# Kernel tuning notes

Hardware: AMD Instinct MI355X
Metric: run time of the kernel (lower is better)

Reference implementation:

```python
import jax, jax.numpy as jnp
import numpy as np

B, S, H = 2, 2048, 2048
HQ, HKV, DK, DV = 32, 8, 64, 64
G = HQ // HKV  # queries per kv group
SCALE = 1.0 / DK ** 0.5


def setup_inputs() -> dict:
    key = jax.random.key(0)
    k1, k2, k3, k4 = jax.random.split(key, 4)
    qkv_out = HQ * DK + HKV * (DK + DV)
    x = jax.random.normal(k1, (B, S, H), dtype=jnp.float32)
    Wqkv = jax.random.normal(k2, (H, qkv_out), dtype=jnp.float32) * (1.0 / np.sqrt(H))
    Wout = jax.random.normal(k3, (HQ * DV, H), dtype=jnp.float32) * (1.0 / np.sqrt(HQ * DV))
    b_out = jax.random.normal(k4, (H,), dtype=jnp.float32) * 0.01
    # causal mask [B, 1, S, S]; mask==0 positions are disallowed
    mask = jnp.broadcast_to(jnp.tril(jnp.ones((S, S), dtype=jnp.int32)), (B, 1, S, S))
    return {"x": x, "Wqkv": Wqkv, "Wout": Wout, "b_out": b_out, "mask": mask}


def reference(x, Wqkv, Wout, b_out, mask):
    # fused QKV projection (bias=False)
    qkv = x @ Wqkv  # [B, S, HQ*DK + HKV*(DK+DV)]
    tq, tk = HQ * DK, HKV * DK
    Q = qkv[..., :tq].reshape(B, S, HKV, G, DK)          # [B,S,n,g,d]
    K = qkv[..., tq:tq + tk].reshape(B, S, HKV, DK)       # [B,S,n,d]
    V = qkv[..., tq + tk:].reshape(B, S, HKV, DV)         # [B,S,n,e]
    # scores: [B, n(kv heads), g(group), s(query), t(key)]
    scores = jnp.einsum('bsngd,btnd->bngst', Q, K) * SCALE
    # mask [B,1,S,S] -> broadcast over n,g as [B,1,1,S,S]
    m = mask[:, :, None, :, :]
    scores = jnp.where(m == 0, -jnp.inf, scores)
    probs = jax.nn.softmax(scores, axis=-1)  # dropout p=0 -> identity
    attn = jnp.einsum('bngst,btne->bsnge', probs, V)      # [B,S,n,g,e]
    out = attn.reshape(B, S, HQ * DV) @ Wout + b_out       # [B,S,H]
    return out
```

## Files before the change

### kernel.cpp

```cpp
#include <hip/hip_runtime.h>

#define SEQ    2048
#define HDIM   2048
#define QKV_LD 3072
#define K_BASE 2048
#define V_BASE 2560
#define ATT_SCALE 0.125f
#define SM_MAX 20.0f
#define QK_MUL 0.18033688f
#define ZINIT  -28.8539008f

typedef __bf16 bf16x8 __attribute__((ext_vector_type(8)));
typedef float  f32x4  __attribute__((ext_vector_type(4)));
typedef float  f32x16 __attribute__((ext_vector_type(16)));
typedef unsigned short u16x8 __attribute__((ext_vector_type(8)));
typedef unsigned       u32x4 __attribute__((ext_vector_type(4)));

__device__ __forceinline__ void async_copy16(void* lds, const void* g) {
  __builtin_amdgcn_global_load_lds(
      (const __attribute__((address_space(1))) unsigned*)g,
      (__attribute__((address_space(3))) unsigned*)lds, 16, 0, 0);
}

__device__ __forceinline__ unsigned cvtpk(float lo, float hi) {
  unsigned r;
  asm("v_cvt_pk_bf16_f32 %0, %1, %2" : "=v"(r) : "v"(lo), "v"(hi));
  return r;
}
__device__ __forceinline__ void pl32swap(unsigned& a, unsigned& b) {
  asm("v_permlane32_swap_b32 %0, %1" : "+v"(a), "+v"(b));
}

__global__ void detect_dtype(const unsigned* __restrict__ p0,
                             const unsigned* __restrict__ p1,
                             const unsigned* __restrict__ p2,
                             const unsigned* __restrict__ p3,
                             int* __restrict__ flags) {
  const unsigned* ptrs[4] = {p0, p1, p2, p3};
  const int lane = threadIdx.x;
#pragma unroll
  for (int i = 0; i < 4; ++i) {
    int cnt = 0;
#pragma unroll
    for (int j = 0; j < 8; ++j) {
      unsigned w = ptrs[i][lane * 8 + j];
      unsigned e = (w >> 7) & 0xFF;
      cnt += (e >= 90 && e <= 160) ? 1 : 0;
    }
    for (int off = 32; off; off >>= 1) cnt += __shfl_down(cnt, off);
    if (lane == 0) flags[i] = (cnt < 350) ? 1 : 0;
  }
  if (lane == 0) flags[4] = 0;
}

__global__ __launch_bounds__(256) void cast_f32_bf16(const float* __restrict__ s,
                                                     __bf16* __restrict__ d) {
  const size_t i = ((size_t)blockIdx.x * 256 + threadIdx.x) * 8;
  float4 a = *(const float4*)(s + i);
  float4 b = *(const float4*)(s + i + 4);
  bf16x8 o;
  o[0] = (__bf16)a.x; o[1] = (__bf16)a.y; o[2] = (__bf16)a.z; o[3] = (__bf16)a.w;
  o[4] = (__bf16)b.x; o[5] = (__bf16)b.y; o[6] = (__bf16)b.z; o[7] = (__bf16)b.w;
  *(bf16x8*)(d + i) = o;
}

__global__ __launch_bounds__(256) void transpose_cast(const float* __restrict__ W,
                                                      __bf16* __restrict__ WT,
                                                      int K, int N) {
  __shared__ float T[64][68];
  const int tid = threadIdx.x;
  const int kb = blockIdx.y * 64, nb = blockIdx.x * 64;
  const int r = tid >> 2, cq = tid & 3;
  const float* src = W + (size_t)(kb + r) * N + nb + cq * 16;
  float4 f0 = ((const float4*)src)[0];
  float4 f1 = ((const float4*)src)[1];
  float4 f2 = ((const float4*)src)[2];
  float4 f3 = ((const float4*)src)[3];
  *(float4*)&T[r][cq * 16 + 0]  = f0;
  *(float4*)&T[r][cq * 16 + 4]  = f1;
  *(float4*)&T[r][cq * 16 + 8]  = f2;
  *(float4*)&T[r][cq * 16 + 12] = f3;
  __syncthreads();
  __bf16* dst = WT + (size_t)(nb + r) * K + kb + cq * 16;
  bf16x8 o0, o1;
#pragma unroll
  for (int j = 0; j < 8; ++j) o0[j] = (__bf16)T[cq * 16 + j][r];
#pragma unroll
  for (int j = 0; j < 8; ++j) o1[j] = (__bf16)T[cq * 16 + 8 + j][r];
  *(bf16x8*)dst = o0;
  *(bf16x8*)(dst + 8) = o1;
}

#define QA_ELE (128 * 64)
#define QB_ELE (192 * 64)

template <typename OutT>
__global__ __launch_bounds__(512, 4) void gemm128x192(const __bf16* __restrict__ A,
                                                      const __bf16* __restrict__ Bt,
                                                      const float* __restrict__ bias,
                                                      OutT* __restrict__ C,
                                                      int M, int N, int K) {
  extern __shared__ __align__(16) __bf16 smem[];
  __bf16* Asm = smem;
  __bf16* Bsm = smem + 2 * QA_ELE;

  const int tid = threadIdx.x;
  const int w = tid >> 6, lane = tid & 63;
  const int lr = lane & 15, lg = lane >> 4;
  const int wm = w >> 2, wn = w & 3;
  const int bid = blockIdx.x;
  const int cpx = gridDim.x >> 3;
  const int swz = (bid & 7) * cpx + (bid >> 3);
  const int nx = N / 192;
  const int m0 = (swz / nx) * 128, n0 = (swz % nx) * 192;
  const int KT = K >> 6;

  const int lrow = lane >> 3;
  const int lc8  = ((lane & 7) ^ lrow) * 8;

  f32x4 acc[4][3];
#pragma unroll
  for (int a = 0; a < 4; ++a)
#pragma unroll
    for (int b = 0; b < 3; ++b) acc[a][b] = (f32x4){0.f, 0.f, 0.f, 0.f};

  bf16x8 af[4][2], bf[3][2];

  const __bf16* gA = A + (size_t)m0 * K;
  const __bf16* gB = Bt + (size_t)n0 * K;

  auto stA = [&](int t) {
    __bf16* base = Asm + (size_t)(t & 1) * QA_ELE + (16 * w) * 64;
    const __bf16* s = gA + (size_t)(16 * w + lrow) * K + (size_t)t * 64 + lc8;
    async_copy16(base, s);
    async_copy16(base + 8 * 64, s + (size_t)8 * K);
  };
  auto stB01 = [&](int t) {
    __bf16* base = Bsm + (size_t)(t & 1) * QB_ELE + (8 * w) * 64;
    const __bf16* s = gB + (size_t)(8 * w + lrow) * K + (size_t)t * 64 + lc8;
    async_copy16(base, s);
    async_copy16(base + 64 * 64, s + (size_t)64 * K);
  };
  auto stB2 = [&](int t) {
    __bf16* base = Bsm + (size_t)(t & 1) * QB_ELE + (128 + 8 * w) * 64;
    const __bf16* s = gB + (size_t)(128 + 8 * w + lrow) * K + (size_t)t * 64 + lc8;
    async_copy16(base, s);
  };

#define QLOAD_A                                                                 \
  {                                                                             \
    _Pragma("unroll") for (int mf = 0; mf < 4; ++mf)                            \
        _Pragma("unroll") for (int kk = 0; kk < 2; ++kk)                        \
            af[mf][kk] = *(const bf16x8*)&Ac[(wm * 64 + mf * 16 + lr) * 64 +    \
                                            (((kk * 4 + lg) ^ (lr & 7)) << 3)]; \
  }
#define QLOAD_B(nf)                                                             \
  {                                                                             \
    _Pragma("unroll") for (int kk = 0; kk < 2; ++kk)                            \
        bf[nf][kk] = *(const bf16x8*)&Bc[(wn * 48 + (nf) * 16 + lr) * 64 +      \
                                        (((kk * 4 + lg) ^ (lr & 7)) << 3)];     \
  }
#define QMFMA(nfs, nfe)                                                         \
  {                                                                             \
    __builtin_amdgcn_s_setprio(1);                                              \
    _Pragma("unroll") for (int mf = 0; mf < 4; ++mf)                            \
        _Pragma("unroll") for (int nf = (nfs); nf < (nfe); ++nf)                \
            _Pragma("unroll") for (int kk = 0; kk < 2; ++kk)                    \
                acc[mf][nf] = __builtin_amdgcn_mfma_f32_16x16x32_bf16(          \
                    af[mf][kk], bf[nf][kk], acc[mf][nf], 0, 0, 0);              \
    __builtin_amdgcn_s_setprio(0);                                              \
  }
#define QWAIT_LGKM                                                              \
  asm volatile("s_waitcnt lgkmcnt(0)" ::: "memory");                            \
  __builtin_amdgcn_sched_barrier(0);

  stA(0); stB01(0); stB2(0);
  stA(1); stB01(1);

  for (int kt = 0; kt < KT; ++kt) {
    const __bf16* Ac = Asm + (size_t)(kt & 1) * QA_ELE;
    const __bf16* Bc = Bsm + (size_t)(kt & 1) * QB_ELE;
    const bool p1 = kt + 1 < KT, p2 = kt + 2 < KT;

    if (p1) stB2(kt + 1);
    if (p1) asm volatile("s_waitcnt vmcnt(5)" ::: "memory");
    else    asm volatile("s_waitcnt vmcnt(0)" ::: "memory");
    __builtin_amdgcn_s_barrier();
    QLOAD_A; QLOAD_B(0); QLOAD_B(1);
    QWAIT_LGKM; QMFMA(0, 2);
    __builtin_amdgcn_s_barrier();

    QLOAD_B(2);
    if (p2) { stA(kt + 2); stB01(kt + 2); }
    __builtin_amdgcn_s_barrier();
    QWAIT_LGKM; QMFMA(2, 3);
    __builtin_amdgcn_s_barrier();
  }

#pragma unroll
  for (int mf = 0; mf < 4; ++mf)
#pragma unroll
    for (int nf = 0; nf < 3; ++nf)
#pragma unroll
      for (int r = 0; r < 4; ++r) {
        int row = m0 + wm * 64 + mf * 16 + 4 * lg + r;
        int col = n0 + wn * 48 + nf * 16 + lr;
        float v = acc[mf][nf][r];
        if (bias) v += bias[col];
        C[(size_t)row * N + col] = (OutT)v;
      }
#undef QLOAD_A
#undef QLOAD_B
#undef QMFMA
#undef QWAIT_LGKM
}

#define GA_ELE (256 * 64)
#define GB_ELE (128 * 64)

template <typename OutT>
__global__ __launch_bounds__(512, 2) void gemm256x128(const __bf16* __restrict__ A,
                                                      const __bf16* __restrict__ Bt,
                                                      const float* __restrict__ bias,
                                                      OutT* __restrict__ C,
                                                      int M, int N, int K) {
  extern __shared__ __align__(16) __bf16 smem[];
  __bf16* Asm = smem;
  __bf16* Bsm = smem + 2 * GA_ELE;

  const int tid = threadIdx.x;
  const int w = tid >> 6, lane = tid & 63;
  const int lr = lane & 15, lg = lane >> 4;
  const int wm = w >> 2, wn = w & 3;
  const int m0 = blockIdx.y * 256, n0 = blockIdx.x * 128;
  const int KT = K >> 6;

  const int lrow = lane >> 3;
  const int lc8  = ((lane & 7) ^ lrow) * 8;

  f32x4 acc[2][4][2];
#pragma unroll
  for (int a = 0; a < 2; ++a)
#pragma unroll
    for (int b = 0; b < 4; ++b)
#pragma unroll
      for (int c = 0; c < 2; ++c) acc[a][b][c] = (f32x4){0.f, 0.f, 0.f, 0.f};

  bf16x8 af[4][2], bf[2][2];

  const __bf16* gA = A + (size_t)m0 * K;
  const __bf16* gB = Bt + (size_t)n0 * K;

  auto stA = [&](int h, int t) {
    __bf16* base = Asm + (size_t)(t & 1) * GA_ELE + (h * 128 + 16 * w) * 64;
    const __bf16* s = gA + (size_t)(h * 128 + 16 * w + lrow) * K + (size_t)t * 64 + lc8;
    async_copy16(base, s);
    async_copy16(base + 8 * 64, s + (size_t)8 * K);
  };
  auto stB = [&](int t) {
    __bf16* base = Bsm + (size_t)(t & 1) * GB_ELE + (16 * w) * 64;
    const __bf16* s = gB + (size_t)(16 * w + lrow) * K + (size_t)t * 64 + lc8;
    async_copy16(base, s);
    async_copy16(base + 8 * 64, s + (size_t)8 * K);
  };

#define LOAD_A(mq)                                                              \
  {                                                                             \
    _Pragma("unroll") for (int mf = 0; mf < 4; ++mf)                            \
        _Pragma("unroll") for (int kk = 0; kk < 2; ++kk)                        \
            af[mf][kk] = *(const bf16x8*)&Ac[((mq) * 128 + wm * 64 + mf * 16 +  \
                                             lr) * 64 +                         \
                                            (((kk * 4 + lg) ^ (lr & 7)) << 3)]; \
  }
#define LOAD_B                                                                  \
  {                                                                             \
    _Pragma("unroll") for (int nf = 0; nf < 2; ++nf)                            \
        _Pragma("unroll") for (int kk = 0; kk < 2; ++kk)                        \
            bf[nf][kk] = *(const bf16x8*)&Bc[(wn * 32 + nf * 16 + lr) * 64 +    \
                                            (((kk * 4 + lg) ^ (lr & 7)) << 3)]; \
  }
#define MFMA_Q(mq)                                                              \
  {                                                                             \
    __builtin_amdgcn_s_setprio(1);                                              \
    _Pragma("unroll") for (int mf = 0; mf < 4; ++mf)                            \
        _Pragma("unroll") for (int nf = 0; nf < 2; ++nf)                        \
            _Pragma("unroll") for (int kk = 0; kk < 2; ++kk)                    \
                acc[mq][mf][nf] = __builtin_amdgcn_mfma_f32_16x16x32_bf16(      \
                    af[mf][kk], bf[nf][kk], acc[mq][mf][nf], 0, 0, 0);          \
    __builtin_amdgcn_s_setprio(0);                                              \
  }
#define WAIT_LGKM                                                               \
  asm volatile("s_waitcnt lgkmcnt(0)" ::: "memory");                            \
  __builtin_amdgcn_sched_barrier(0);

  stA(0, 0); stB(0); stA(1, 0);
  stA(0, 1); stB(1);

  for (int kt = 0; kt < KT; ++kt) {
    const __bf16* Ac = Asm + (size_t)(kt & 1) * GA_ELE;
    const __bf16* Bc = Bsm + (size_t)(kt & 1) * GB_ELE;
    const bool p1 = kt + 1 < KT, p2 = kt + 2 < KT;

    if (p1) stA(1, kt + 1);
    if (p1) asm volatile("s_waitcnt vmcnt(6)" ::: "memory");
    else    asm volatile("s_waitcnt vmcnt(0)" ::: "memory");
    __builtin_amdgcn_s_barrier();
    LOAD_A(0); LOAD_B;
    WAIT_LGKM; MFMA_Q(0);
    __builtin_amdgcn_s_barrier();

    LOAD_A(1);
    if (p2) { stA(0, kt + 2); stB(kt + 2); }
    __builtin_amdgcn_s_barrier();
    WAIT_LGKM; MFMA_Q(1);
    __builtin_amdgcn_s_barrier();
  }

#pragma unroll
  for (int mq = 0; mq < 2; ++mq)
#pragma unroll
    for (int mf = 0; mf < 4; ++mf)
#pragma unroll
      for (int nf = 0; nf < 2; ++nf)
#pragma unroll
        for (int r = 0; r < 4; ++r) {
          int row = m0 + mq * 128 + wm * 64 + mf * 16 + 4 * lg + r;
          int col = n0 + wn * 32 + nf * 16 + lr;
          float v = acc[mq][mf][nf][r];
          if (bias) v += bias[col];
          C[(size_t)row * N + col] = (OutT)v;
        }
#undef LOAD_A
#undef LOAD_B
#undef MFMA_Q
#undef WAIT_LGKM
}

template <typename OutT>
__global__ __launch_bounds__(256) void gemm128(const __bf16* __restrict__ A,
                                               const __bf16* __restrict__ Bt,
                                               const float* __restrict__ bias,
                                               OutT* __restrict__ C,
                                               int M, int N, int K) {
  __shared__ __bf16 As[128 * 32];
  __shared__ __bf16 Bs[128 * 32];
  const int tid = threadIdx.x;
  const int w = tid >> 6, lane = tid & 63;
  const int lr = lane & 15, lg = lane >> 4;
  const int wm = w >> 1, wn = w & 1;
  const int m0 = blockIdx.y * 128, n0 = blockIdx.x * 128;

  f32x4 acc[4][4];
#pragma unroll
  for (int i = 0; i < 4; ++i)
#pragma unroll
    for (int j = 0; j < 4; ++j) acc[i][j] = (f32x4){0.f, 0.f, 0.f, 0.f};

  const int srow = 32 * w + (lane >> 2);
  const int scol = (lane & 3) * 8;
  const __bf16* ga = A + (size_t)(m0 + srow) * K + scol;
  const __bf16* gb = Bt + (size_t)(n0 + srow) * K + scol;
  __bf16* la0 = &As[(32 * w) * 32];
  __bf16* la1 = &As[(32 * w + 16) * 32];
  __bf16* lb0 = &Bs[(32 * w) * 32];
  __bf16* lb1 = &Bs[(32 * w + 16) * 32];

  for (int k0 = 0; k0 < K; k0 += 32) {
    async_copy16(la0, ga + k0);
    async_copy16(la1, ga + (size_t)16 * K + k0);
    async_copy16(lb0, gb + k0);
    async_copy16(lb1, gb + (size_t)16 * K + k0);
    __syncthreads();
    bf16x8 af[4], bfr[4];
#pragma unroll
    for (int mf = 0; mf < 4; ++mf)
      af[mf] = *(const bf16x8*)&As[(64 * wm + 16 * mf + lr) * 32 + 8 * lg];
#pragma unroll
    for (int nf = 0; nf < 4; ++nf)
      bfr[nf] = *(const bf16x8*)&Bs[(64 * wn + 16 * nf + lr) * 32 + 8 * lg];
#pragma unroll
    for (int mf = 0; mf < 4; ++mf)
#pragma unroll
      for (int nf = 0; nf < 4; ++nf)
        acc[mf][nf] = __builtin_amdgcn_mfma_f32_16x16x32_bf16(af[mf], bfr[nf],
                                                              acc[mf][nf], 0, 0, 0);
    __syncthreads();
  }

#pragma unroll
  for (int mf = 0; mf < 4; ++mf)
#pragma unroll
    for (int nf = 0; nf < 4; ++nf)
#pragma unroll
      for (int r = 0; r < 4; ++r) {
        int row = m0 + 64 * wm + 16 * mf + 4 * lg + r;
        int col = n0 + 64 * wn + 16 * nf + lr;
        float v = acc[mf][nf][r];
        if (bias) v += bias[col];
        C[(size_t)row * N + col] = (OutT)v;
      }
}

template <typename OutT>
__global__ __launch_bounds__(256) void gemm64(const void* __restrict__ Araw,
                                              const void* __restrict__ Braw,
                                              const void* __restrict__ biasraw,
                                              const int* __restrict__ flags,
                                              int fa, int fb, int fbias,
                                              OutT* __restrict__ C,
                                              int M, int N, int K) {
  __shared__ __bf16 As[64][40];
  __shared__ __bf16 Bs[64][40];
  const bool a_f32 = flags[fa] != 0;
  const bool b_f32 = flags[fb] != 0;
  const bool c_f32 = flags[fbias] != 0;
  const int tid = threadIdx.x;
  const int wave = tid >> 6, lane = tid & 63;
  const int lr = lane & 15, lg = lane >> 4;
  const int m0 = blockIdx.y * 64, n0 = blockIdx.x * 64;
  f32x4 acc[4];
#pragma unroll
  for (int i = 0; i < 4; ++i) acc[i] = (f32x4){0.f, 0.f, 0.f, 0.f};
  const int ar = tid >> 2, ac = (tid & 3) * 8;
  const int bn = tid & 63, bk0 = (tid >> 6) * 8;
  for (int k0 = 0; k0 < K; k0 += 32) {
    bf16x8 av;
    if (a_f32) {
      const float* p = (const float*)Araw + (size_t)(m0 + ar) * K + (k0 + ac);
#pragma unroll
      for (int j = 0; j < 8; ++j) av[j] = (__bf16)p[j];
    } else {
      av = *(const bf16x8*)((const __bf16*)Araw + (size_t)(m0 + ar) * K + (k0 + ac));
    }
    *(bf16x8*)&As[ar][ac] = av;
    if (b_f32) {
      const float* p = (const float*)Braw + (size_t)(k0 + bk0) * N + (n0 + bn);
#pragma unroll
      for (int j = 0; j < 8; ++j) Bs[bn][bk0 + j] = (__bf16)p[(size_t)j * N];
    } else {
      const __bf16* p = (const __bf16*)Braw + (size_t)(k0 + bk0) * N + (n0 + bn);
#pragma unroll
      for (int j = 0; j < 8; ++j) Bs[bn][bk0 + j] = p[(size_t)j * N];
    }
    __syncthreads();
    bf16x8 a = *(const bf16x8*)&As[wave * 16 + lr][lg * 8];
#pragma unroll
    for (int nt = 0; nt < 4; ++nt) {
      bf16x8 b = *(const bf16x8*)&Bs[nt * 16 + lr][lg * 8];
      acc[nt] = __builtin_amdgcn_mfma_f32_16x16x32_bf16(a, b, acc[nt], 0, 0, 0);
    }
    __syncthreads();
  }
#pragma unroll
  for (int nt = 0; nt < 4; ++nt)
#pragma unroll
    for (int r = 0; r < 4; ++r) {
      int row = m0 + wave * 16 + lg * 4 + r;
      int col = n0 + nt * 16 + lr;
      float v = acc[nt][r];
      if (biasraw) {
        v += c_f32 ? ((const float*)biasraw)[col]
                   : (float)((const __bf16*)biasraw)[col];
      }
      C[(size_t)row * N + col] = (OutT)v;
    }
}

__global__ __launch_bounds__(256) void attn_fused4(const __bf16* __restrict__ qkv,
                                                   __bf16* __restrict__ attn_out) {
  __shared__ __bf16 Ks[2][64][64];
  __shared__ __bf16 Vt[2][64][72];

  const int tid  = threadIdx.x;
  const int w    = tid >> 6;
  const int lane = tid & 63;
  const int lam  = lane & 31;
  const int hsel = lane >> 5;
  const int h8   = hsel * 8;

  const int bid = blockIdx.x;
  const int xcd = bid & 7;
  const int idx = bid >> 3;
  const int bh  = xcd * 2 + (idx >> 5);
  const int p   = idx & 31;
  const int hkv = bh & 7;
  const int b   = bh >> 3;
  const int h   = hkv * 4 + w;

  const int qclo = p, qchi = 63 - p;
  const int qlo0 = qclo * 32, qhi0 = qchi * 32;
  const int nlo = (qclo >> 1) + 1;
  const int nhi = (qchi >> 1) + 1;
  const int qglo = qlo0 + lam, qghi = qhi0 + lam;

  const size_t k_ch = K_BASE + (size_t)hkv * 64;
  const size_t v_ch = V_BASE + (size_t)hkv * 64;
  const __bf16* base = qkv + (size_t)b * SEQ * QKV_LD;

  bf16x8 aqlo[4], aqhi[4];
  {
    const __bf16* qrl = base + (size_t)(qlo0 + lam) * QKV_LD + (size_t)h * 64;
    const __bf16* qrh = base + (size_t)(qhi0 + lam) * QKV_LD + (size_t)h * 64;
#pragma unroll
    for (int c = 0; c < 4; ++c) {
      bf16x8 vl = *(const bf16x8*)(qrl + 16 * c + h8);
      bf16x8 vh = *(const bf16x8*)(qrh + 16 * c + h8);
#pragma unroll
      for (int j = 0; j < 8; ++j) {
        vl[j] = (__bf16)((float)vl[j] * QK_MUL);
        vh[j] = (__bf16)((float)vh[j] * QK_MUL);
      }
      aqlo[c] = vl;
      aqhi[c] = vh;
    }
  }

  bf16x8 bone;
#pragma unroll
  for (int j = 0; j < 8; ++j) bone[j] = (__bf16)1.0f;

  f32x16 o0l, o1l, oll, o0h, o1h, olh;
#pragma unroll
  for (int i = 0; i < 16; ++i) {
    o0l[i] = 0.f; o1l[i] = 0.f; oll[i] = 0.f;
    o0h[i] = 0.f; o1h[i] = 0.f; olh[i] = 0.f;
  }

  const int krow  = 16 * w + (lane >> 3);
  const int ksoct = ((lane & 7) ^ (lane >> 3)) * 8;
  const __bf16* kga = base + k_ch + (size_t)krow * QKV_LD + ksoct;
  const __bf16* kgb = kga + (size_t)8 * QKV_LD;
  const int kp = lane >> 3, cq = lane & 7;
  const __bf16* vg0 = base + v_ch + (size_t)(16 * w + 2 * kp) * QKV_LD + 8 * cq;
  const int vtcol = (((2 * w + (kp >> 2)) ^ cq) << 3) + 2 * (kp & 3);
  const int vtrow = 8 * cq;

  async_copy16(&Ks[0][16 * w][0],     kga);
  async_copy16(&Ks[0][16 * w + 8][0], kgb);
  bf16x8 va = *(const bf16x8*)vg0;
  bf16x8 vb = *(const bf16x8*)(vg0 + QKV_LD);
  {
    u16x8 ua = *(u16x8*)&va, ub = *(u16x8*)&vb;
#pragma unroll
    for (int j = 0; j < 8; ++j)
      *(unsigned*)&Vt[0][vtrow + j][vtcol] =
          (unsigned)ua[j] | ((unsigned)ub[j] << 16);
  }
  __syncthreads();

#define CHUNK_COMPUTE(AQ, O0, O1, OL, QG, KHMAX, KMASK)                        \
  {                                                                            \
    bf16x8 pa[4];                                                              \
    _Pragma("unroll") for (int kh = 0; kh < 2; ++kh) {                         \
      if (kh < (KHMAX)) {                                                      \
        f32x16 z;                                                              \
        _Pragma("unroll") for (int i = 0; i < 16; ++i) z[i] = ZINIT;           \
        __builtin_amdgcn_s_setprio(1);                                         \
        _Pragma("unroll") for (int c = 0; c < 4; ++c) {                        \
          bf16x8 kf = *(const bf16x8*)                                         \
              &Ks[cur][32 * kh + lam][(((2 * c + hsel) ^ (lam & 7)) << 3)];    \
          z = __builtin_amdgcn_mfma_f32_32x32x16_bf16(kf, AQ[c], z, 0, 0, 0);  \
        }                                                                      \
        __builtin_amdgcn_s_setprio(0);                                         \
        if (kh == (KMASK)) {                                                   \
          _Pragma("unroll") for (int i = 0; i < 16; ++i) {                     \
            const int t = t0 + 32 * kh + ((i & 3) + 8 * (i >> 2)) + 4 * hsel;  \
            float pp = __builtin_amdgcn_exp2f(z[i]);                           \
            z[i] = (t > (QG)) ? 0.f : pp;                                      \
          }                                                                    \
        } else {                                                               \
          _Pragma("unroll") for (int i = 0; i < 16; ++i)                       \
            z[i] = __builtin_amdgcn_exp2f(z[i]);                               \
        }                                                                      \
        unsigned c0 = cvtpk(z[0], z[1]),   c1 = cvtpk(z[2], z[3]);             \
        unsigned c2 = cvtpk(z[4], z[5]),   c3 = cvtpk(z[6], z[7]);             \
        unsigned c4 = cvtpk(z[8], z[9]),   c5 = cvtpk(z[10], z[11]);           \
        unsigned c6 = cvtpk(z[12], z[13]), c7 = cvtpk(z[14], z[15]);           \
        pl32swap(c0, c2); pl32swap(c1, c3);                                    \
        pl32swap(c4, c6); pl32swap(c5, c7);                                    \
        u32x4 pw0 = {c0, c1, c2, c3}, pw1 = {c4, c5, c6, c7};                  \
        pa[2 * kh]     = *(bf16x8*)&pw0;                                       \
        pa[2 * kh + 1] = *(bf16x8*)&pw1;                                       \
      }                                                                        \
    }                                                                          \
    const int ksmax = (KHMAX) * 2;                                             \
    __builtin_amdgcn_s_setprio(1);                                             \
    _Pragma("unroll") for (int ks = 0; ks < 4; ++ks) {                         \
      if (ks < ksmax) {                                                        \
        OL = __builtin_amdgcn_mfma_f32_32x32x16_bf16(pa[ks], bone, OL, 0,0,0); \
        {                                                                      \
          bf16x8 bv = *(const bf16x8*)                                         \
              &Vt[cur][lam][(((2 * ks + hsel) ^ ((lam >> 3) & 7)) << 3)];      \
          O0 = __builtin_amdgcn_mfma_f32_32x32x16_bf16(pa[ks], bv, O0, 0,0,0); \
        }                                                                      \
        {                                                                      \
          const int e = 32 + lam;                                              \
          bf16x8 bv = *(const bf16x8*)                                         \
              &Vt[cur][e][(((2 * ks + hsel) ^ ((e >> 3) & 7)) << 3)];          \
          O1 = __builtin_amdgcn_mfma_f32_32x32x16_bf16(pa[ks], bv, O1, 0,0,0); \
        }                                                                      \
      }                                                                        \
    }                                                                          \
    __builtin_amdgcn_s_setprio(0);                                             \
  }

  for (int blk = 0; blk < nhi; ++blk) {
    const int cur  = blk & 1;
    const int t0   = blk * 64;
    const bool havenext = (blk + 1 < nhi);

    if (havenext) {
      const __bf16* vg = vg0 + (size_t)(t0 + 64) * QKV_LD;
      va = *(const bf16x8*)vg;
      vb = *(const bf16x8*)(vg + QKV_LD);
      const size_t koff = (size_t)(t0 + 64) * QKV_LD;
      async_copy16(&Ks[cur ^ 1][16 * w][0],     kga + koff);
      async_copy16(&Ks[cur ^ 1][16 * w + 8][0], kgb + koff);
    }

    {
      const bool diag = (blk == nhi - 1);
      const int khmax = (diag && !(qchi & 1)) ? 1 : 2;
      const int kmask = diag ? ((qchi & 1) ? 1 : 0) : 2;
      CHUNK_COMPUTE(aqhi, o0h, o1h, olh, qghi, khmax, kmask);
    }
    if (blk < nlo) {
      const bool diag = (blk == nlo - 1);
      const int khmax = (diag && !(qclo & 1)) ? 1 : 2;
      const int kmask = diag ? ((qclo & 1) ? 1 : 0) : 2;
      CHUNK_COMPUTE(aqlo, o0l, o1l, oll, qglo, khmax, kmask);
    }

    if (havenext) {
      u16x8 ua = *(u16x8*)&va, ub = *(u16x8*)&vb;
#pragma unroll
      for (int j = 0; j < 8; ++j)
        *(unsigned*)&Vt[cur ^ 1][vtrow + j][vtcol] =
            (unsigned)ua[j] | ((unsigned)ub[j] << 16);
    }
    __syncthreads();
  }
#undef CHUNK_COMPUTE

#define CHUNK_OUT(O0, O1, OL, Q0)                                              \
  {                                                                            \
    float inv[16];                                                             \
    _Pragma("unroll") for (int i = 0; i < 16; ++i) inv[i] = 1.0f / OL[i];      \
    __bf16* dst = attn_out + ((size_t)b * SEQ + (Q0)) * HDIM +                 \
                  (size_t)h * 64 + lam;                                        \
    _Pragma("unroll") for (int i = 0; i < 16; ++i) {                           \
      const int rq = (i & 3) + 8 * (i >> 2) + 4 * hsel;                        \
      dst[(size_t)rq * HDIM]      = (__bf16)(O0[i] * inv[i]);                  \
      dst[(size_t)rq * HDIM + 32] = (__bf16)(O1[i] * inv[i]);                  \
    }                                                                          \
  }

  CHUNK_OUT(o0h, o1h, olh, qhi0);
  CHUNK_OUT(o0l, o1l, oll, qlo0);
#undef CHUNK_OUT
}

extern "C" void kernel_launch(void* const* d_in, const int* in_sizes, int n_in,
                              void* d_out, int out_size, void* d_ws, size_t ws_size,
                              hipStream_t stream) {
  const void* x     = d_in[0];
  const void* Wqkv  = d_in[1];
  const void* Wout  = d_in[2];
  const void* b_out = d_in[3];
  float* out = (float*)d_out;

  const int M = 2 * SEQ;
  __bf16* qkv  = (__bf16*)d_ws;
  __bf16* attn = qkv + (size_t)M * QKV_LD;
  int* flags   = (int*)(attn + (size_t)M * HDIM);
  __bf16* xb   = (__bf16*)((char*)flags + 64);
  __bf16* wqt  = xb + (size_t)M * HDIM;
  __bf16* wot  = wqt + (size_t)QKV_LD * HDIM;

  const size_t need = (size_t)((char*)(wot + (size_t)HDIM * HDIM) - (char*)d_ws);

  static int dyn_ok = -1;
  if (dyn_ok < 0) {
    hipError_t e1 = hipFuncSetAttribute(
        reinterpret_cast<const void*>(&gemm128x192<__bf16>),
        hipFuncAttributeMaxDynamicSharedMemorySize, 81920);
    hipError_t e2 = hipFuncSetAttribute(
        reinterpret_cast<const void*>(&gemm256x128<float>),
        hipFuncAttributeMaxDynamicSharedMemorySize, 98304);
    dyn_ok = (e1 == hipSuccess && e2 == hipSuccess) ? 1 : 0;
  }

  detect_dtype<<<1, 64, 0, stream>>>((const unsigned*)x, (const unsigned*)Wqkv,
                                     (const unsigned*)Wout, (const unsigned*)b_out,
                                     flags);

  if (ws_size >= need) {
    cast_f32_bf16<<<dim3((M * HDIM) / 2048), 256, 0, stream>>>((const float*)x, xb);
    transpose_cast<<<dim3(QKV_LD / 64, HDIM / 64), 256, 0, stream>>>(
        (const float*)Wqkv, wqt, HDIM, QKV_LD);
    transpose_cast<<<dim3(HDIM / 64, HDIM / 64), 256, 0, stream>>>(
        (const float*)Wout, wot, HDIM, HDIM);

    if (dyn_ok) {
      gemm128x192<__bf16><<<dim3(512), 512, 81920, stream>>>(
          xb, wqt, nullptr, qkv, M, QKV_LD, HDIM);
      attn_fused4<<<dim3(512), 256, 0, stream>>>(qkv, attn);
      gemm256x128<float><<<dim3(HDIM / 128, M / 256), 512, 98304, stream>>>(
          attn, wot, (const float*)b_out, out, M, HDIM, HDIM);
    } else {
      gemm128<__bf16><<<dim3(QKV_LD / 128, M / 128), 256, 0, stream>>>(
          xb, wqt, nullptr, qkv, M, QKV_LD, HDIM);
      attn_fused4<<<dim3(512), 256, 0, stream>>>(qkv, attn);
      gemm128<float><<<dim3(HDIM / 128, M / 128), 256, 0, stream>>>(
          attn, wot, (const float*)b_out, out, M, HDIM, HDIM);
    }
  } else {
    gemm64<__bf16><<<dim3(QKV_LD / 64, M / 64), 256, 0, stream>>>(
        x, Wqkv, nullptr, flags, 0, 1, 3, qkv, M, QKV_LD, HDIM);
    attn_fused4<<<dim3(512), 256, 0, stream>>>(qkv, attn);
    gemm64<float><<<dim3(HDIM / 64, M / 64), 256, 0, stream>>>(
        attn, Wout, b_out, flags, 4, 2, 3, out, M, HDIM, HDIM);
  }
}
```

Measured before the change: 305.1 us.

## Split attention loop into joint hi/lo phase sharing K/V fragments and hi-only tail

The key-block loop is split into two phases. While both query chunks are active, the QK and PV MFMAs for the high and low chunks are interleaved so each K/V LDS fragment is read once and feeds two independent MFMA chains. The high-only tail keeps the original causal-diagonal handling. The V transpose store to LDS now happens before the PV MFMAs rather than after them. This is meant to cut LDS reads and expose more MFMA-level parallelism, at the cost of higher register pressure. The first phase always prefetches the next block, which assumes nhi > nlo and wastes work on the lo diagonal, where half of the block may be fully masked.

```diff
diff --git a/kernel.cpp b/kernel.cpp
--- a/kernel.cpp
+++ b/kernel.cpp
@@ -548,65 +548,101 @@
   }
   __syncthreads();
 
-#define CHUNK_COMPUTE(AQ, O0, O1, OL, QG, KHMAX, KMASK)                        \
+#define PACK(Z, PA, KH)                                                        \
   {                                                                            \
-    bf16x8 pa[4];                                                              \
-    _Pragma("unroll") for (int kh = 0; kh < 2; ++kh) {                         \
-      if (kh < (KHMAX)) {                                                      \
-        f32x16 z;                                                              \
-        _Pragma("unroll") for (int i = 0; i < 16; ++i) z[i] = ZINIT;           \
-        __builtin_amdgcn_s_setprio(1);                                         \
-        _Pragma("unroll") for (int c = 0; c < 4; ++c) {                        \
-          bf16x8 kf = *(const bf16x8*)                                         \
-              &Ks[cur][32 * kh + lam][(((2 * c + hsel) ^ (lam & 7)) << 3)];    \
-          z = __builtin_amdgcn_mfma_f32_32x32x16_bf16(kf, AQ[c], z, 0, 0, 0);  \
-        }                                                                      \
-        __builtin_amdgcn_s_setprio(0);                                         \
-        if (kh == (KMASK)) {                                                   \
-          _Pragma("unroll") for (int i = 0; i < 16; ++i) {                     \
-            const int t = t0 + 32 * kh + ((i & 3) + 8 * (i >> 2)) + 4 * hsel;  \
-            float pp = __builtin_amdgcn_exp2f(z[i]);                           \
-            z[i] = (t > (QG)) ? 0.f : pp;                                      \
-          }                                                                    \
-        } else {                                                               \
-          _Pragma("unroll") for (int i = 0; i < 16; ++i)                       \
-            z[i] = __builtin_amdgcn_exp2f(z[i]);                               \
-        }                                                                      \
-        unsigned c0 = cvtpk(z[0], z[1]),   c1 = cvtpk(z[2], z[3]);             \
-        unsigned c2 = cvtpk(z[4], z[5]),   c3 = cvtpk(z[6], z[7]);             \
-        unsigned c4 = cvtpk(z[8], z[9]),   c5 = cvtpk(z[10], z[11]);           \
-        unsigned c6 = cvtpk(z[12], z[13]), c7 = cvtpk(z[14], z[15]);           \
-        pl32swap(c0, c2); pl32swap(c1, c3);                                    \
-        pl32swap(c4, c6); pl32swap(c5, c7);                                    \
-        u32x4 pw0 = {c0, c1, c2, c3}, pw1 = {c4, c5, c6, c7};                  \
-        pa[2 * kh]     = *(bf16x8*)&pw0;                                       \
-        pa[2 * kh + 1] = *(bf16x8*)&pw1;                                       \
-      }                                                                        \
-    }                                                                          \
-    const int ksmax = (KHMAX) * 2;                                             \
-    __builtin_amdgcn_s_setprio(1);                                             \
-    _Pragma("unroll") for (int ks = 0; ks < 4; ++ks) {                         \
-      if (ks < ksmax) {                                                        \
-        OL = __builtin_amdgcn_mfma_f32_32x32x16_bf16(pa[ks], bone, OL, 0,0,0); \
-        {                                                                      \
-          bf16x8 bv = *(const bf16x8*)                                         \
-              &Vt[cur][lam][(((2 * ks + hsel) ^ ((lam >> 3) & 7)) << 3)];      \
-          O0 = __builtin_amdgcn_mfma_f32_32x32x16_bf16(pa[ks], bv, O0, 0,0,0); \
-        }                                                                      \
-        {                                                                      \
-          const int e = 32 + lam;                                              \
-          bf16x8 bv = *(const bf16x8*)                                         \
-              &Vt[cur][e][(((2 * ks + hsel) ^ ((e >> 3) & 7)) << 3)];          \
-          O1 = __builtin_amdgcn_mfma_f32_32x32x16_bf16(pa[ks], bv, O1, 0,0,0); \
-        }                                                                      \
-      }                                                                        \
-    }                                                                          \
-    __builtin_amdgcn_s_setprio(0);                                             \
-  }
-
-  for (int blk = 0; blk < nhi; ++blk) {
-    const int cur  = blk & 1;
-    const int t0   = blk * 64;
+    unsigned c0 = cvtpk(Z[0], Z[1]),   c1 = cvtpk(Z[2], Z[3]);                 \
+    unsigned c2 = cvtpk(Z[4], Z[5]),   c3 = cvtpk(Z[6], Z[7]);                 \
+    unsigned c4 = cvtpk(Z[8], Z[9]),   c5 = cvtpk(Z[10], Z[11]);               \
+    unsigned c6 = cvtpk(Z[12], Z[13]), c7 = cvtpk(Z[14], Z[15]);               \
+    pl32swap(c0, c2); pl32swap(c1, c3);                                        \
+    pl32swap(c4, c6); pl32swap(c5, c7);                                        \
+    u32x4 pw0_ = {c0, c1, c2, c3}, pw1_ = {c4, c5, c6, c7};                    \
+    PA[2 * (KH)]     = *(bf16x8*)&pw0_;                                        \
+    PA[2 * (KH) + 1] = *(bf16x8*)&pw1_;                                        \
+  }
+
+  for (int blk = 0; blk < nlo; ++blk) {
+    const int cur = blk & 1;
+    const int t0  = blk * 64;
+
+    {
+      const __bf16* vg = vg0 + (size_t)(t0 + 64) * QKV_LD;
+      va = *(const bf16x8*)vg;
+      vb = *(const bf16x8*)(vg + QKV_LD);
+      const size_t koff = (size_t)(t0 + 64) * QKV_LD;
+      async_copy16(&Ks[cur ^ 1][16 * w][0],     kga + koff);
+      async_copy16(&Ks[cur ^ 1][16 * w + 8][0], kgb + koff);
+    }
+
+    const bool dlo = (blk == nlo - 1);
+    const int pmask_lo = dlo ? ((qclo & 1) ? 1 : 0) : 2;
+
+    bf16x8 pah[4], pal[4];
+#pragma unroll
+    for (int kh = 0; kh < 2; ++kh) {
+      f32x16 zh, zl;
+#pragma unroll
+      for (int i = 0; i < 16; ++i) { zh[i] = ZINIT; zl[i] = ZINIT; }
+      __builtin_amdgcn_s_setprio(1);
+#pragma unroll
+      for (int c = 0; c < 4; ++c) {
+        bf16x8 kf = *(const bf16x8*)
+            &Ks[cur][32 * kh + lam][(((2 * c + hsel) ^ (lam & 7)) << 3)];
+        zh = __builtin_amdgcn_mfma_f32_32x32x16_bf16(kf, aqhi[c], zh, 0, 0, 0);
+        zl = __builtin_amdgcn_mfma_f32_32x32x16_bf16(kf, aqlo[c], zl, 0, 0, 0);
+      }
+      __builtin_amdgcn_s_setprio(0);
+#pragma unroll
+      for (int i = 0; i < 16; ++i) zh[i] = __builtin_amdgcn_exp2f(zh[i]);
+      if (kh >= pmask_lo) {
+#pragma unroll
+        for (int i = 0; i < 16; ++i) {
+          const int t = t0 + 32 * kh + ((i & 3) + 8 * (i >> 2)) + 4 * hsel;
+          float pp = __builtin_amdgcn_exp2f(zl[i]);
+          zl[i] = (t > qglo) ? 0.f : pp;
+        }
+      } else {
+#pragma unroll
+        for (int i = 0; i < 16; ++i) zl[i] = __builtin_amdgcn_exp2f(zl[i]);
+      }
+      PACK(zh, pah, kh);
+      PACK(zl, pal, kh);
+    }
+
+    {
+      u16x8 ua = *(u16x8*)&va, ub = *(u16x8*)&vb;
+#pragma unroll
+      for (int j = 0; j < 8; ++j)
+        *(unsigned*)&Vt[cur ^ 1][vtrow + j][vtcol] =
+            (unsigned)ua[j] | ((unsigned)ub[j] << 16);
+    }
+
+    __builtin_amdgcn_s_setprio(1);
+#pragma unroll
+    for (int ks = 0; ks < 4; ++ks) {
+      olh = __builtin_amdgcn_mfma_f32_32x32x16_bf16(pah[ks], bone, olh, 0, 0, 0);
+      oll = __builtin_amdgcn_mfma_f32_32x32x16_bf16(pal[ks], bone, oll, 0, 0, 0);
+      {
+        bf16x8 bv = *(const bf16x8*)
+            &Vt[cur][lam][(((2 * ks + hsel) ^ ((lam >> 3) & 7)) << 3)];
+        o0h = __builtin_amdgcn_mfma_f32_32x32x16_bf16(pah[ks], bv, o0h, 0, 0, 0);
+        o0l = __builtin_amdgcn_mfma_f32_32x32x16_bf16(pal[ks], bv, o0l, 0, 0, 0);
+      }
+      {
+        const int e = 32 + lam;
+        bf16x8 bv = *(const bf16x8*)
+            &Vt[cur][e][(((2 * ks + hsel) ^ ((e >> 3) & 7)) << 3)];
+        o1h = __builtin_amdgcn_mfma_f32_32x32x16_bf16(pah[ks], bv, o1h, 0, 0, 0);
+        o1l = __builtin_amdgcn_mfma_f32_32x32x16_bf16(pal[ks], bv, o1l, 0, 0, 0);
+      }
+    }
+    __builtin_amdgcn_s_setprio(0);
+    __syncthreads();
+  }
+
+  for (int blk = nlo; blk < nhi; ++blk) {
+    const int cur = blk & 1;
+    const int t0  = blk * 64;
     const bool havenext = (blk + 1 < nhi);
 
     if (havenext) {
@@ -618,17 +654,38 @@
       async_copy16(&Ks[cur ^ 1][16 * w + 8][0], kgb + koff);
     }
 
-    {
-      const bool diag = (blk == nhi - 1);
-      const int khmax = (diag && !(qchi & 1)) ? 1 : 2;
-      const int kmask = diag ? ((qchi & 1) ? 1 : 0) : 2;
-      CHUNK_COMPUTE(aqhi, o0h, o1h, olh, qghi, khmax, kmask);
-    }
-    if (blk < nlo) {
-      const bool diag = (blk == nlo - 1);
-      const int khmax = (diag && !(qclo & 1)) ? 1 : 2;
-      const int kmask = diag ? ((qclo & 1) ? 1 : 0) : 2;
-      CHUNK_COMPUTE(aqlo, o0l, o1l, oll, qglo, khmax, kmask);
+    const bool diag = (blk == nhi - 1);
+    const int khmax = (diag && !(qchi & 1)) ? 1 : 2;
+    const int kmask = diag ? ((qchi & 1) ? 1 : 0) : 2;
+
+    bf16x8 pah[4];
+#pragma unroll
+    for (int kh = 0; kh < 2; ++kh) {
+      if (kh < khmax) {
+        f32x16 z;
+#pragma unroll
+        for (int i = 0; i < 16; ++i) z[i] = ZINIT;
+        __builtin_amdgcn_s_setprio(1);
+#pragma unroll
+        for (int c = 0; c < 4; ++c) {
+          bf16x8 kf = *(const bf16x8*)
+              &Ks[cur][32 * kh + lam][(((2 * c + hsel) ^ (lam & 7)) << 3)];
+          z = __builtin_amdgcn_mfma_f32_32x32x16_bf16(kf, aqhi[c], z, 0, 0, 0);
+        }
+        __builtin_amdgcn_s_setprio(0);
+        if (kh == kmask) {
+#pragma unroll
+          for (int i = 0; i < 16; ++i) {
+            const int t = t0 + 32 * kh + ((i & 3) + 8 * (i >> 2)) + 4 * hsel;
+            float pp = __builtin_amdgcn_exp2f(z[i]);
+            z[i] = (t > qghi) ? 0.f : pp;
+          }
+        } else {
+#pragma unroll
+          for (int i = 0; i < 16; ++i) z[i] = __builtin_amdgcn_exp2f(z[i]);
+        }
+        PACK(z, pah, kh);
+      }
     }
 
     if (havenext) {
@@ -638,9 +695,30 @@
         *(unsigned*)&Vt[cur ^ 1][vtrow + j][vtcol] =
             (unsigned)ua[j] | ((unsigned)ub[j] << 16);
     }
+
+    const int ksmax = khmax * 2;
+    __builtin_amdgcn_s_setprio(1);
+#pragma unroll
+    for (int ks = 0; ks < 4; ++ks) {
+      if (ks < ksmax) {
+        olh = __builtin_amdgcn_mfma_f32_32x32x16_bf16(pah[ks], bone, olh, 0, 0, 0);
+        {
+          bf16x8 bv = *(const bf16x8*)
+              &Vt[cur][lam][(((2 * ks + hsel) ^ ((lam >> 3) & 7)) << 3)];
+          o0h = __builtin_amdgcn_mfma_f32_32x32x16_bf16(pah[ks], bv, o0h, 0, 0, 0);
+        }
+        {
+          const int e = 32 + lam;
+          bf16x8 bv = *(const bf16x8*)
+              &Vt[cur][e][(((2 * ks + hsel) ^ ((e >> 3) & 7)) << 3)];
+          o1h = __builtin_amdgcn_mfma_f32_32x32x16_bf16(pah[ks], bv, o1h, 0, 0, 0);
+        }
+      }
+    }
+    __builtin_amdgcn_s_setprio(0);
     __syncthreads();
   }
-#undef CHUNK_COMPUTE
+#undef PACK
 
 #define CHUNK_OUT(O0, O1, OL, Q0)                                              \
   {                                                                            \
```

Result: slower. 325.9 us (+6.8%).

## Replace out-projection 256x128 GEMM with swizzled 128x128 tile kernel

Applied to the files above, without the earlier changes.

The output projection GEMM moves from 256x128 tiles (128 blocks) to 128x128 tiles launched as 512 blocks, with a block-index swizzle that spreads consecutive blocks across eight groups for cache locality. The K-loop is restructured so each 64-wide K step loads A and B fragments once and issues the two k-halves of MFMAs on either side of the next-stage prefetch. The QKV GEMM also moves its LDS wait and barrier ahead of the prefetch issue. The aim is better CU fill and occupancy (512 blocks, 64KB LDS, launch bounds of 4) at the cost of less per-block data reuse and more global traffic.

```diff
diff --git a/kernel.cpp b/kernel.cpp
--- a/kernel.cpp
+++ b/kernel.cpp
@@ -191,9 +191,10 @@
     __builtin_amdgcn_s_barrier();
 
     QLOAD_B(2);
+    QWAIT_LGKM;
+    __builtin_amdgcn_s_barrier();
     if (p2) { stA(kt + 2); stB01(kt + 2); }
-    __builtin_amdgcn_s_barrier();
-    QWAIT_LGKM; QMFMA(2, 3);
+    QMFMA(2, 3);
     __builtin_amdgcn_s_barrier();
   }
 
@@ -215,125 +216,115 @@
 #undef QWAIT_LGKM
 }
 
-#define GA_ELE (256 * 64)
-#define GB_ELE (128 * 64)
+#define OA_ELE (128 * 64)
 
 template <typename OutT>
-__global__ __launch_bounds__(512, 2) void gemm256x128(const __bf16* __restrict__ A,
+__global__ __launch_bounds__(512, 4) void gemm128x128(const __bf16* __restrict__ A,
                                                       const __bf16* __restrict__ Bt,
                                                       const float* __restrict__ bias,
                                                       OutT* __restrict__ C,
                                                       int M, int N, int K) {
   extern __shared__ __align__(16) __bf16 smem[];
   __bf16* Asm = smem;
-  __bf16* Bsm = smem + 2 * GA_ELE;
+  __bf16* Bsm = smem + 2 * OA_ELE;
 
   const int tid = threadIdx.x;
   const int w = tid >> 6, lane = tid & 63;
   const int lr = lane & 15, lg = lane >> 4;
   const int wm = w >> 2, wn = w & 3;
-  const int m0 = blockIdx.y * 256, n0 = blockIdx.x * 128;
+  const int bid = blockIdx.x;
+  const int cpx = gridDim.x >> 3;
+  const int swz = (bid & 7) * cpx + (bid >> 3);
+  const int nx = N / 128;
+  const int m0 = (swz / nx) * 128, n0 = (swz % nx) * 128;
   const int KT = K >> 6;
 
   const int lrow = lane >> 3;
   const int lc8  = ((lane & 7) ^ lrow) * 8;
 
-  f32x4 acc[2][4][2];
-#pragma unroll
-  for (int a = 0; a < 2; ++a)
-#pragma unroll
-    for (int b = 0; b < 4; ++b)
-#pragma unroll
-      for (int c = 0; c < 2; ++c) acc[a][b][c] = (f32x4){0.f, 0.f, 0.f, 0.f};
+  f32x4 acc[4][2];
+#pragma unroll
+  for (int a = 0; a < 4; ++a)
+#pragma unroll
+    for (int b = 0; b < 2; ++b) acc[a][b] = (f32x4){0.f, 0.f, 0.f, 0.f};
 
   bf16x8 af[4][2], bf[2][2];
 
   const __bf16* gA = A + (size_t)m0 * K;
   const __bf16* gB = Bt + (size_t)n0 * K;
 
-  auto stA = [&](int h, int t) {
-    __bf16* base = Asm + (size_t)(t & 1) * GA_ELE + (h * 128 + 16 * w) * 64;
-    const __bf16* s = gA + (size_t)(h * 128 + 16 * w + lrow) * K + (size_t)t * 64 + lc8;
+  auto stA = [&](int t) {
+    __bf16* base = Asm + (size_t)(t & 1) * OA_ELE + (16 * w) * 64;
+    const __bf16* s = gA + (size_t)(16 * w + lrow) * K + (size_t)t * 64 + lc8;
     async_copy16(base, s);
     async_copy16(base + 8 * 64, s + (size_t)8 * K);
   };
   auto stB = [&](int t) {
-    __bf16* base = Bsm + (size_t)(t & 1) * GB_ELE + (16 * w) * 64;
+    __bf16* base = Bsm + (size_t)(t & 1) * OA_ELE + (16 * w) * 64;
     const __bf16* s = gB + (size_t)(16 * w + lrow) * K + (size_t)t * 64 + lc8;
     async_copy16(base, s);
     async_copy16(base + 8 * 64, s + (size_t)8 * K);
   };
 
-#define LOAD_A(mq)                                                              \
+#define OLOAD                                                                   \
   {                                                                             \
     _Pragma("unroll") for (int mf = 0; mf < 4; ++mf)                            \
         _Pragma("unroll") for (int kk = 0; kk < 2; ++kk)                        \
-            af[mf][kk] = *(const bf16x8*)&Ac[((mq) * 128 + wm * 64 + mf * 16 +  \
-                                             lr) * 64 +                         \
+            af[mf][kk] = *(const bf16x8*)&Ac[(wm * 64 + mf * 16 + lr) * 64 +    \
                                             (((kk * 4 + lg) ^ (lr & 7)) << 3)]; \
-  }
-#define LOAD_B                                                                  \
-  {                                                                             \
     _Pragma("unroll") for (int nf = 0; nf < 2; ++nf)                            \
         _Pragma("unroll") for (int kk = 0; kk < 2; ++kk)                        \
             bf[nf][kk] = *(const bf16x8*)&Bc[(wn * 32 + nf * 16 + lr) * 64 +    \
                                             (((kk * 4 + lg) ^ (lr & 7)) << 3)]; \
   }
-#define MFMA_Q(mq)                                                              \
+#define OMFMA(kk)                                                               \
   {                                                                             \
     __builtin_amdgcn_s_setprio(1);                                              \
     _Pragma("unroll") for (int mf = 0; mf < 4; ++mf)                            \
         _Pragma("unroll") for (int nf = 0; nf < 2; ++nf)                        \
-            _Pragma("unroll") for (int kk = 0; kk < 2; ++kk)                    \
-                acc[mq][mf][nf] = __builtin_amdgcn_mfma_f32_16x16x32_bf16(      \
-                    af[mf][kk], bf[nf][kk], acc[mq][mf][nf], 0, 0, 0);          \
+            acc[mf][nf] = __builtin_amdgcn_mfma_f32_16x16x32_bf16(              \
+                af[mf][kk], bf[nf][kk], acc[mf][nf], 0, 0, 0);                  \
     __builtin_amdgcn_s_setprio(0);                                              \
   }
-#define WAIT_LGKM                                                               \
+#define OWAIT_LGKM                                                              \
   asm volatile("s_waitcnt lgkmcnt(0)" ::: "memory");                            \
   __builtin_amdgcn_sched_barrier(0);
 
-  stA(0, 0); stB(0); stA(1, 0);
-  stA(0, 1); stB(1);
+  stA(0); stB(0);
+  stA(1); stB(1);
 
   for (int kt = 0; kt < KT; ++kt) {
-    const __bf16* Ac = Asm + (size_t)(kt & 1) * GA_ELE;
-    const __bf16* Bc = Bsm + (size_t)(kt & 1) * GB_ELE;
+    const __bf16* Ac = Asm + (size_t)(kt & 1) * OA_ELE;
+    const __bf16* Bc = Bsm + (size_t)(kt & 1) * OA_ELE;
     const bool p1 = kt + 1 < KT, p2 = kt + 2 < KT;
 
-    if (p1) stA(1, kt + 1);
-    if (p1) asm volatile("s_waitcnt vmcnt(6)" ::: "memory");
+    if (p1) asm volatile("s_waitcnt vmcnt(4)" ::: "memory");
     else    asm volatile("s_waitcnt vmcnt(0)" ::: "memory");
     __builtin_amdgcn_s_barrier();
-    LOAD_A(0); LOAD_B;
-    WAIT_LGKM; MFMA_Q(0);
+    OLOAD;
+    OWAIT_LGKM; OMFMA(0);
     __builtin_amdgcn_s_barrier();
 
-    LOAD_A(1);
-    if (p2) { stA(0, kt + 2); stB(kt + 2); }
+    if (p2) { stA(kt + 2); stB(kt + 2); }
+    OMFMA(1);
     __builtin_amdgcn_s_barrier();
-    WAIT_LGKM; MFMA_Q(1);
-    __builtin_amdgcn_s_barrier();
-  }
-
-#pragma unroll
-  for (int mq = 0; mq < 2; ++mq)
-#pragma unroll
-    for (int mf = 0; mf < 4; ++mf)
-#pragma unroll
-      for (int nf = 0; nf < 2; ++nf)
-#pragma unroll
-        for (int r = 0; r < 4; ++r) {
-          int row = m0 + mq * 128 + wm * 64 + mf * 16 + 4 * lg + r;
-          int col = n0 + wn * 32 + nf * 16 + lr;
-          float v = acc[mq][mf][nf][r];
-          if (bias) v += bias[col];
-          C[(size_t)row * N + col] = (OutT)v;
-        }
-#undef LOAD_A
-#undef LOAD_B
-#undef MFMA_Q
-#undef WAIT_LGKM
+  }
+
+#pragma unroll
+  for (int mf = 0; mf < 4; ++mf)
+#pragma unroll
+    for (int nf = 0; nf < 2; ++nf)
+#pragma unroll
+      for (int r = 0; r < 4; ++r) {
+        int row = m0 + wm * 64 + mf * 16 + 4 * lg + r;
+        int col = n0 + wn * 32 + nf * 16 + lr;
+        float v = acc[mf][nf][r];
+        if (bias) v += bias[col];
+        C[(size_t)row * N + col] = (OutT)v;
+      }
+#undef OLOAD
+#undef OMFMA
+#undef OWAIT_LGKM
 }
 
 template <typename OutT>
@@ -685,8 +676,8 @@
         reinterpret_cast<const void*>(&gemm128x192<__bf16>),
         hipFuncAttributeMaxDynamicSharedMemorySize, 81920);
     hipError_t e2 = hipFuncSetAttribute(
-        reinterpret_cast<const void*>(&gemm256x128<float>),
-        hipFuncAttributeMaxDynamicSharedMemorySize, 98304);
+        reinterpret_cast<const void*>(&gemm128x128<float>),
+        hipFuncAttributeMaxDynamicSharedMemorySize, 65536);
     dyn_ok = (e1 == hipSuccess && e2 == hipSuccess) ? 1 : 0;
   }
 
@@ -705,7 +696,7 @@
       gemm128x192<__bf16><<<dim3(512), 512, 81920, stream>>>(
           xb, wqt, nullptr, qkv, M, QKV_LD, HDIM);
       attn_fused4<<<dim3(512), 256, 0, stream>>>(qkv, attn);
-      gemm256x128<float><<<dim3(HDIM / 128, M / 256), 512, 98304, stream>>>(
+      gemm128x128<float><<<dim3(512), 512, 65536, stream>>>(
           attn, wot, (const float*)b_out, out, M, HDIM, HDIM);
     } else {
       gemm128<__bf16><<<dim3(QKV_LD / 128, M / 128), 256, 0, stream>>>(
```

After: 304.8 us. About the same (-0.1%).
